# Kernel optimization log

Measured on AMD Instinct MI355X. Metric: run time of the kernel, lower is better.

Reference implementation:

```python
import jax, jax.numpy as jnp
import numpy as np
from jax import lax

T, IN_DIM, H = 8192, 512, 1024


def setup_inputs() -> dict:
    key = jax.random.key(0)
    ks = jax.random.split(key, 6)
    def lin(k, fan_in, shape):
        return jax.random.normal(k, shape, dtype=jnp.float32) / np.sqrt(fan_in)
    return {
        "x": jax.random.normal(ks[0], (T, IN_DIM), dtype=jnp.float32),
        "W_ih_0": lin(ks[1], IN_DIM, (IN_DIM, 4 * H)),
        "W_hh_0": lin(ks[2], H, (H, 4 * H)),
        "b_0": jnp.zeros((4 * H,), dtype=jnp.float32),
        "W_ih_1": lin(ks[3], H, (H, 4 * H)),
        "W_hh_1": lin(ks[4], H, (H, 4 * H)),
        "b_1": jnp.zeros((4 * H,), dtype=jnp.float32),
    }


def _lstm_layer(inp, W_ih, W_hh, b):
    """inp: (T, D) -> hiddens (T, H). Input projection batched across all T."""
    hdim = W_hh.shape[0]
    xg = inp @ W_ih  # (T, 4H), all-timestep GEMM

    def step(carry, xg_t):
        h, c = carry
        gates = xg_t + h @ W_hh + b  # (4H,)
        i, f, g, o = jnp.split(gates, 4, axis=-1)
        i = jax.nn.sigmoid(i)
        f = jax.nn.sigmoid(f)
        g = jnp.tanh(g)
        o = jax.nn.sigmoid(o)
        new_c = f * c + i * g
        new_h = o * jnp.tanh(new_c)
        return (new_h, new_c), new_h

    init = (jnp.zeros((hdim,), inp.dtype), jnp.zeros((hdim,), inp.dtype))
    _, hiddens = lax.scan(step, init, xg)
    return hiddens  # (T, H)


def reference(x, W_ih_0, W_hh_0, b_0, W_ih_1, W_hh_1, b_1):
    h1 = _lstm_layer(x, W_ih_0, W_hh_0, b_0)
    h2 = _lstm_layer(h1, W_ih_1, W_hh_1, b_1)
    return h2
```

## Files before the change

### kernel.cpp

```cpp
#include <hip/hip_runtime.h>
#include <stdint.h>


#define TT    8192
#define INDIM 512
#define HH    1024
#define G4    4096
#define NBLK  256

#define SENT 0x7FC00000u

typedef float    f32x4 __attribute__((ext_vector_type(4)));
typedef uint32_t u32x4 __attribute__((ext_vector_type(4)));

__device__ __forceinline__ float sigf(float x) { return 1.0f / (1.0f + __expf(-x)); }

__global__ void fill4_kernel(float* __restrict__ p, long n4, uint32_t pat) {
  float pv = __uint_as_float(pat);
  f32x4 v = { pv, pv, pv, pv };
  long i = (long)blockIdx.x * blockDim.x + threadIdx.x;
  long stride = (long)gridDim.x * blockDim.x;
  for (; i < n4; i += stride) {
    const float* a = p + i * 4;
    asm volatile("global_store_dwordx4 %0, %1, off sc0 sc1" :: "v"(a), "v"(v) : "memory");
  }
}

__global__ __launch_bounds__(256, 2) void gemm_bias_f32(
    const float* __restrict__ A, const float* __restrict__ B,
    const float* __restrict__ bias, float* __restrict__ C,
    int M, int N, int K)
{
  constexpr int BM = 128, BN = 128, BK = 16, TM = 8, TN = 8;
  __shared__ float As[BK][BM];
  __shared__ float Bs[BK][BN];
  const int tid = threadIdx.x;
  const int bm = blockIdx.y * BM;
  const int bn = blockIdx.x * BN;
  const int tm = (tid >> 4) * TM;
  const int tn = (tid & 15) * TN;
  float acc[TM][TN] = {};
  for (int k0 = 0; k0 < K; k0 += BK) {
    #pragma unroll
    for (int i = 0; i < 2; ++i) {
      int idx = tid * 2 + i;
      int r = idx >> 2, c4 = idx & 3;
      float4 a = *(const float4*)(A + (size_t)(bm + r) * K + k0 + c4 * 4);
      As[c4 * 4 + 0][r] = a.x;
      As[c4 * 4 + 1][r] = a.y;
      As[c4 * 4 + 2][r] = a.z;
      As[c4 * 4 + 3][r] = a.w;
    }
    #pragma unroll
    for (int i = 0; i < 2; ++i) {
      int idx = tid * 2 + i;
      int r = idx >> 5, c4 = idx & 31;
      *(float4*)&Bs[r][c4 * 4] = *(const float4*)(B + (size_t)(k0 + r) * N + bn + c4 * 4);
    }
    __syncthreads();
    #pragma unroll
    for (int kk = 0; kk < BK; ++kk) {
      float ar[TM], br[TN];
      *(float4*)&ar[0] = *(const float4*)&As[kk][tm];
      *(float4*)&ar[4] = *(const float4*)&As[kk][tm + 4];
      *(float4*)&br[0] = *(const float4*)&Bs[kk][tn];
      *(float4*)&br[4] = *(const float4*)&Bs[kk][tn + 4];
      #pragma unroll
      for (int i = 0; i < TM; ++i)
        #pragma unroll
        for (int j = 0; j < TN; ++j)
          acc[i][j] = fmaf(ar[i], br[j], acc[i][j]);
    }
    __syncthreads();
  }
  #pragma unroll
  for (int i = 0; i < TM; ++i) {
    float* crow = C + (size_t)(bm + tm + i) * N + bn + tn;
    #pragma unroll
    for (int j = 0; j < TN; j += 4) {
      float4 v;
      v.x = acc[i][j + 0] + bias[bn + tn + j + 0];
      v.y = acc[i][j + 1] + bias[bn + tn + j + 1];
      v.z = acc[i][j + 2] + bias[bn + tn + j + 2];
      v.w = acc[i][j + 3] + bias[bn + tn + j + 3];
      *(float4*)(crow + j) = v;
    }
  }
}

__global__ __launch_bounds__(256, 1) void lstm_scan_kernel(
    const float* __restrict__ xg,
    const float* __restrict__ Whh,
    float* __restrict__ hout,
    uint32_t* __restrict__ flags,
    uint32_t fval, int nsteps)
{
  __shared__ float hsh[HH];
  const int tid = threadIdx.x;
  const int w = tid >> 6;
  const int l = tid & 63;
  const int g = l >> 4;
  const int p = l & 15;
  const int u = blockIdx.x * 4 + w;
  const int col = g * HH + u;

  float wr[64];
  #pragma unroll
  for (int k = 0; k < 16; ++k)
    #pragma unroll
    for (int e = 0; e < 4; ++e)
      wr[4 * k + e] = Whh[(size_t)(4 * (p + 16 * k) + e) * G4 + col];

  float c = 0.0f;
  float xgv = xg[col];
  uint32_t budget = (1u << 20);

  for (int t = 0; t < nsteps; ++t) {
    float xg_cur = xgv;
    int tnx = (t + 1 < nsteps) ? t + 1 : t;
    xgv = xg[(size_t)tnx * G4 + col];

    float red = 0.0f;
    if (t > 0) {
      if (w == 0) {
        const uint32_t* fa = flags + (size_t)(t - 1) * NBLK + l * 4;
        int fdone = 0;
        do {
          u32x4 f;
          asm volatile("global_load_dwordx4 %0, %1, off sc0 sc1"
                       : "=v"(f) : "v"(fa));
          asm volatile("s_waitcnt vmcnt(0)" ::: "memory");
          __builtin_amdgcn_sched_barrier(0);
          int valid = (f.x >= fval) & (f.y >= fval) & (f.z >= fval) & (f.w >= fval);
          fdone = __all(valid);
          if (!fdone) { --budget; asm volatile("s_sleep 1"); }
        } while (!fdone && budget);
      }
      __syncthreads();

      {
        const float* ha = hout + (size_t)(t - 1) * HH + tid * 4;
        f32x4 hvv;
        int hd = 0;
        do {
          asm volatile("global_load_dwordx4 %0, %1, off sc0 sc1"
                       : "=v"(hvv) : "v"(ha));
          asm volatile("s_waitcnt vmcnt(0)" ::: "memory");
          __builtin_amdgcn_sched_barrier(0);
          hd = (__float_as_uint(hvv.x) != SENT) & (__float_as_uint(hvv.y) != SENT)
             & (__float_as_uint(hvv.z) != SENT) & (__float_as_uint(hvv.w) != SENT);
          if (!hd) --budget;
        } while (!hd && budget);
        if (!hd) {
          if (__float_as_uint(hvv.x) == SENT) hvv.x = 0.0f;
          if (__float_as_uint(hvv.y) == SENT) hvv.y = 0.0f;
          if (__float_as_uint(hvv.z) == SENT) hvv.z = 0.0f;
          if (__float_as_uint(hvv.w) == SENT) hvv.w = 0.0f;
        }
        *(f32x4*)&hsh[tid * 4] = hvv;
      }
      __syncthreads();

      float s0 = 0.f, s1 = 0.f, s2 = 0.f, s3 = 0.f;
      #pragma unroll
      for (int k = 0; k < 16; ++k) {
        f32x4 hk = *(const f32x4*)&hsh[p * 4 + 64 * k];
        s0 = fmaf(wr[4 * k + 0], hk.x, s0);
        s1 = fmaf(wr[4 * k + 1], hk.y, s1);
        s2 = fmaf(wr[4 * k + 2], hk.z, s2);
        s3 = fmaf(wr[4 * k + 3], hk.w, s3);
      }
      red = (s0 + s1) + (s2 + s3);
      #pragma unroll
      for (int m = 1; m < 16; m <<= 1) red += __shfl_xor(red, m, 64);
    }

    float gp = red + xg_cur;
    float gi_ = __shfl(gp, 0, 64);
    float gf_ = __shfl(gp, 16, 64);
    float gg_ = __shfl(gp, 32, 64);
    float go_ = __shfl(gp, 48, 64);
    float iv = sigf(gi_);
    float fv = sigf(gf_);
    float gv = tanhf(gg_);
    float ov = sigf(go_);
    c = fv * c + iv * gv;
    float h = ov * tanhf(c);
    if (l == 0) {
      __hip_atomic_store(hout + (size_t)t * HH + u, h,
                         __ATOMIC_RELAXED, __HIP_MEMORY_SCOPE_SYSTEM);
    }
    __syncthreads();
    if (tid == 0) {
      __hip_atomic_store(flags + (size_t)t * NBLK + blockIdx.x, fval,
                         __ATOMIC_RELAXED, __HIP_MEMORY_SCOPE_SYSTEM);
    }
  }
}

extern "C" void kernel_launch(void* const* d_in, const int* in_sizes, int n_in,
                              void* d_out, int out_size, void* d_ws, size_t ws_size,
                              hipStream_t stream)
{
  const float* x    = (const float*)d_in[0];
  const float* Wih0 = (const float*)d_in[1];
  const float* Whh0 = (const float*)d_in[2];
  const float* b0   = (const float*)d_in[3];
  const float* Wih1 = (const float*)d_in[4];
  const float* Whh1 = (const float*)d_in[5];
  const float* b1   = (const float*)d_in[6];
  float* out = (float*)d_out;

  float* ws    = (float*)d_ws;
  float* xgbuf = ws;
  float* h1    = ws + (size_t)TT * G4;
  uint32_t* flags = (uint32_t*)(ws + (size_t)TT * G4 + (size_t)TT * HH);

  fill4_kernel<<<2048, 256, 0, stream>>>(h1, (long)TT * HH / 4, SENT);
  fill4_kernel<<<2048, 256, 0, stream>>>(out, (long)TT * HH / 4, SENT);
  fill4_kernel<<<2048, 256, 0, stream>>>((float*)flags, (long)TT * NBLK / 4, 0u);

  dim3 gblk(256);
  dim3 ggrid(G4 / 128, TT / 128);

  gemm_bias_f32<<<ggrid, gblk, 0, stream>>>(x, Wih0, b0, xgbuf, TT, G4, INDIM);
  lstm_scan_kernel<<<NBLK, 256, 0, stream>>>(xgbuf, Whh0, h1, flags, 1u, TT);
  gemm_bias_f32<<<ggrid, gblk, 0, stream>>>(h1, Wih1, b1, xgbuf, TT, G4, HH);
  lstm_scan_kernel<<<NBLK, 256, 0, stream>>>(xgbuf, Whh1, out, flags, 2u, TT);
}
```

Before: 40.01 ms.

## Replace per-block flag barrier with direct sentinel polling on hidden state

Removes the separate per-step flag array and its store/poll protocol. Each thread now spins directly on its slice of the previous step's hidden vector until no element still holds the NaN sentinel. This drops one global round trip, one block barrier per step, and the flag fill kernel from the serial critical path. Correctness now rests only on the sentinel values written by the hidden-state stores.

```diff
diff --git a/kernel.cpp b/kernel.cpp
--- a/kernel.cpp
+++ b/kernel.cpp
@@ -10,8 +10,7 @@
 
 #define SENT 0x7FC00000u
 
-typedef float    f32x4 __attribute__((ext_vector_type(4)));
-typedef uint32_t u32x4 __attribute__((ext_vector_type(4)));
+typedef float f32x4 __attribute__((ext_vector_type(4)));
 
 __device__ __forceinline__ float sigf(float x) { return 1.0f / (1.0f + __expf(-x)); }
 
@@ -92,8 +91,7 @@
     const float* __restrict__ xg,
     const float* __restrict__ Whh,
     float* __restrict__ hout,
-    uint32_t* __restrict__ flags,
-    uint32_t fval, int nsteps)
+    int nsteps)
 {
   __shared__ float hsh[HH];
   const int tid = threadIdx.x;
@@ -122,43 +120,26 @@
 
     float red = 0.0f;
     if (t > 0) {
-      if (w == 0) {
-        const uint32_t* fa = flags + (size_t)(t - 1) * NBLK + l * 4;
-        int fdone = 0;
-        do {
-          u32x4 f;
-          asm volatile("global_load_dwordx4 %0, %1, off sc0 sc1"
-                       : "=v"(f) : "v"(fa));
-          asm volatile("s_waitcnt vmcnt(0)" ::: "memory");
-          __builtin_amdgcn_sched_barrier(0);
-          int valid = (f.x >= fval) & (f.y >= fval) & (f.z >= fval) & (f.w >= fval);
-          fdone = __all(valid);
-          if (!fdone) { --budget; asm volatile("s_sleep 1"); }
-        } while (!fdone && budget);
+      const float* ha = hout + (size_t)(t - 1) * HH + tid * 4;
+      f32x4 hvv;
+      int hd = 0;
+      do {
+        asm volatile("global_load_dwordx4 %0, %1, off sc0 sc1"
+                     : "=v"(hvv) : "v"(ha));
+        asm volatile("s_waitcnt vmcnt(0)" ::: "memory");
+        __builtin_amdgcn_sched_barrier(0);
+        hd = (__float_as_uint(hvv.x) != SENT) & (__float_as_uint(hvv.y) != SENT)
+           & (__float_as_uint(hvv.z) != SENT) & (__float_as_uint(hvv.w) != SENT);
+        if (!hd) --budget;
+      } while (!hd && budget);
+      if (!hd) {
+        if (__float_as_uint(hvv.x) == SENT) hvv.x = 0.0f;
+        if (__float_as_uint(hvv.y) == SENT) hvv.y = 0.0f;
+        if (__float_as_uint(hvv.z) == SENT) hvv.z = 0.0f;
+        if (__float_as_uint(hvv.w) == SENT) hvv.w = 0.0f;
       }
       __syncthreads();
-
-      {
-        const float* ha = hout + (size_t)(t - 1) * HH + tid * 4;
-        f32x4 hvv;
-        int hd = 0;
-        do {
-          asm volatile("global_load_dwordx4 %0, %1, off sc0 sc1"
-                       : "=v"(hvv) : "v"(ha));
-          asm volatile("s_waitcnt vmcnt(0)" ::: "memory");
-          __builtin_amdgcn_sched_barrier(0);
-          hd = (__float_as_uint(hvv.x) != SENT) & (__float_as_uint(hvv.y) != SENT)
-             & (__float_as_uint(hvv.z) != SENT) & (__float_as_uint(hvv.w) != SENT);
-          if (!hd) --budget;
-        } while (!hd && budget);
-        if (!hd) {
-          if (__float_as_uint(hvv.x) == SENT) hvv.x = 0.0f;
-          if (__float_as_uint(hvv.y) == SENT) hvv.y = 0.0f;
-          if (__float_as_uint(hvv.z) == SENT) hvv.z = 0.0f;
-          if (__float_as_uint(hvv.w) == SENT) hvv.w = 0.0f;
-        }
-        *(f32x4*)&hsh[tid * 4] = hvv;
-      }
+      *(f32x4*)&hsh[tid * 4] = hvv;
       __syncthreads();
 
       float s0 = 0.f, s1 = 0.f, s2 = 0.f, s3 = 0.f;
@@ -190,11 +171,6 @@
       __hip_atomic_store(hout + (size_t)t * HH + u, h,
                          __ATOMIC_RELAXED, __HIP_MEMORY_SCOPE_SYSTEM);
     }
-    __syncthreads();
-    if (tid == 0) {
-      __hip_atomic_store(flags + (size_t)t * NBLK + blockIdx.x, fval,
-                         __ATOMIC_RELAXED, __HIP_MEMORY_SCOPE_SYSTEM);
-    }
   }
 }
 
@@ -214,17 +190,15 @@
   float* ws    = (float*)d_ws;
   float* xgbuf = ws;
   float* h1    = ws + (size_t)TT * G4;
-  uint32_t* flags = (uint32_t*)(ws + (size_t)TT * G4 + (size_t)TT * HH);
 
   fill4_kernel<<<2048, 256, 0, stream>>>(h1, (long)TT * HH / 4, SENT);
   fill4_kernel<<<2048, 256, 0, stream>>>(out, (long)TT * HH / 4, SENT);
-  fill4_kernel<<<2048, 256, 0, stream>>>((float*)flags, (long)TT * NBLK / 4, 0u);
 
   dim3 gblk(256);
   dim3 ggrid(G4 / 128, TT / 128);
 
   gemm_bias_f32<<<ggrid, gblk, 0, stream>>>(x, Wih0, b0, xgbuf, TT, G4, INDIM);
-  lstm_scan_kernel<<<NBLK, 256, 0, stream>>>(xgbuf, Whh0, h1, flags, 1u, TT);
+  lstm_scan_kernel<<<NBLK, 256, 0, stream>>>(xgbuf, Whh0, h1, TT);
   gemm_bias_f32<<<ggrid, gblk, 0, stream>>>(h1, Wih1, b1, xgbuf, TT, G4, HH);
-  lstm_scan_kernel<<<NBLK, 256, 0, stream>>>(xgbuf, Whh1, out, flags, 2u, TT);
-}
+  lstm_scan_kernel<<<NBLK, 256, 0, stream>>>(xgbuf, Whh1, out, TT);
+}
```

Result: faster. 38.65 ms (-3.4%).
